# Performance work log

Measured on AMD Instinct MI355X. Metric: run time of the kernel, lower is better.

The kernel has to match this reference:

```python
import jax, jax.numpy as jnp
import numpy as np
import math

HIDDEN = 768
HEADS = 12
HEAD_DIM = HIDDEN // HEADS
B, S = 2, 4096


def setup_inputs() -> dict:
    key = jax.random.key(0)
    ks = jax.random.split(key, 12)
    scale = 1.0 / math.sqrt(HIDDEN)
    inp = {
        "key": jax.random.normal(ks[0], (B, S, HIDDEN), jnp.float32),
        "value": jax.random.normal(ks[1], (B, S, HIDDEN), jnp.float32),
        "query": jax.random.normal(ks[2], (B, S, HIDDEN), jnp.float32),
        "mask": jnp.zeros((B, 1, S, S), jnp.float32),
        # weights stored as [in, out] so projection is x @ W + b
        "Wq": jax.random.normal(ks[3], (HIDDEN, HIDDEN), jnp.float32) * scale,
        "bq": jnp.zeros((HIDDEN,), jnp.float32),
        "Wk": jax.random.normal(ks[4], (HIDDEN, HIDDEN), jnp.float32) * scale,
        "bk": jnp.zeros((HIDDEN,), jnp.float32),
        "Wv": jax.random.normal(ks[5], (HIDDEN, HIDDEN), jnp.float32) * scale,
        "bv": jnp.zeros((HIDDEN,), jnp.float32),
        "Wo": jax.random.normal(ks[6], (HIDDEN, HIDDEN), jnp.float32) * scale,
        "bo": jnp.zeros((HIDDEN,), jnp.float32),
    }
    return inp


def reference(key, value, query, mask, Wq, bq, Wk, bk, Wv, bv, Wo, bo):
    b, s, h = key.shape
    def proj(x, W, bias):
        # [b,s,h] -> [b, heads, s, head_dim]
        y = jnp.dot(x, W) + bias
        return y.reshape(b, s, HEADS, HEAD_DIM).transpose(0, 2, 1, 3)

    q = proj(query, Wq, bq)
    k = proj(key, Wk, bk)
    v = proj(value, Wv, bv)

    inv_sqrt_d = 1.0 / math.sqrt(float(HEAD_DIM))
    scores = jnp.einsum("bnqd,bnkd->bnqk", q, k) * inv_sqrt_d + mask
    probs = jax.nn.softmax(scores, axis=-1)  # dropout p=0.0 -> identity
    ctx = jnp.einsum("bnqk,bnkd->bnqd", probs, v)
    ctx = ctx.transpose(0, 2, 1, 3).reshape(b, s, h)
    return jnp.dot(ctx, Wo) + bo
```

## Files before the change

### kernel.cpp

```cpp
#include <hip/hip_runtime.h>
#include <hip/hip_bf16.h>

#define HID 768
#define NH 12
#define HD 64
#define BB 2
#define SS 4096
#define MM (BB*SS)

typedef unsigned short u16;
typedef __attribute__((ext_vector_type(8))) short short8;
typedef __attribute__((ext_vector_type(8))) unsigned short u16x8;
typedef __attribute__((ext_vector_type(4))) float f32x4;
typedef __attribute__((ext_vector_type(16))) float f32x16;

__device__ __forceinline__ u16 f2bf(float f) {
  union { float f; unsigned u; } v; v.f = f;
  return (u16)((v.u + 0x7fffu + ((v.u >> 16) & 1u)) >> 16);
}

__device__ __forceinline__ unsigned cvtpk(float lo, float hi) {
  unsigned r;
  asm("v_cvt_pk_bf16_f32 %0, %1, %2" : "=v"(r) : "v"(lo), "v"(hi));
  return r;
}

__device__ __forceinline__ short8 mk8(unsigned a, unsigned b, unsigned c, unsigned d) {
  union { unsigned u[4]; short8 s; } x;
  x.u[0] = a; x.u[1] = b; x.u[2] = c; x.u[3] = d;
  return x.s;
}

__global__ void mask_scan(const uint4* __restrict__ m, long long n4, int* __restrict__ flag) {
  long long i = (long long)blockIdx.x * blockDim.x + threadIdx.x;
  long long stride = (long long)gridDim.x * blockDim.x;
  unsigned acc = 0;
  for (; i < n4; i += stride) {
    uint4 v = m[i];
    acc |= v.x | v.y | v.z | v.w;
  }
  if (__any(acc != 0)) {
    if ((threadIdx.x & 63) == 0) atomicOr(flag, 1);
  }
}

__global__ void w_transpose(const float* __restrict__ w0, const float* __restrict__ w1,
                            const float* __restrict__ w2, const float* __restrict__ w3,
                            u16* __restrict__ wt) {
  const float* W = (blockIdx.z == 0) ? w0 : (blockIdx.z == 1) ? w1 : (blockIdx.z == 2) ? w2 : w3;
  u16* Wt = wt + (size_t)blockIdx.z * HID * HID;
  __shared__ float tile[64][65];
  int kb = blockIdx.x * 64, nb = blockIdx.y * 64;
  int t = threadIdx.x;
  int r = t >> 2, cg = (t & 3) << 4;
  const float* src = W + (size_t)(kb + r) * HID + nb + cg;
#pragma unroll
  for (int i = 0; i < 4; i++) {
    float4 v = *(const float4*)(src + 4 * i);
    tile[r][cg + 4*i + 0] = v.x;
    tile[r][cg + 4*i + 1] = v.y;
    tile[r][cg + 4*i + 2] = v.z;
    tile[r][cg + 4*i + 3] = v.w;
  }
  __syncthreads();
  u16x8 a, b;
#pragma unroll
  for (int i = 0; i < 8; i++) a[i] = f2bf(tile[cg + i][r]);
#pragma unroll
  for (int i = 0; i < 8; i++) b[i] = f2bf(tile[cg + 8 + i][r]);
  u16* dst = Wt + (size_t)(nb + r) * HID + kb + cg;
  *(u16x8*)dst = a;
  *(u16x8*)(dst + 8) = b;
}

__global__ void v_transpose(const u16* __restrict__ v_bf, u16* __restrict__ vt_bf) {
  int bh = blockIdx.y, sb = blockIdx.x * 64;
  __shared__ u16 tile[64][72];
  const u16* src = v_bf + (size_t)bh * SS * HD;
  u16* dst = vt_bf + (size_t)bh * HD * SS;
  int t = threadIdx.x;
  int r = t >> 2, cg = (t & 3) << 4;
  *(u16x8*)(&tile[r][cg])     = *(const u16x8*)(src + (size_t)(sb + r) * HD + cg);
  *(u16x8*)(&tile[r][cg + 8]) = *(const u16x8*)(src + (size_t)(sb + r) * HD + cg + 8);
  __syncthreads();
  u16x8 a, b;
#pragma unroll
  for (int i = 0; i < 8; i++) a[i] = tile[cg + i][r];
#pragma unroll
  for (int i = 0; i < 8; i++) b[i] = tile[cg + 8 + i][r];
  *(u16x8*)(dst + (size_t)r * SS + sb + cg) = a;
  *(u16x8*)(dst + (size_t)r * SS + sb + cg + 8) = b;
}

__launch_bounds__(256)
__global__ void proj_qkv(const float* __restrict__ Xq, const float* __restrict__ Xk,
                         const float* __restrict__ Xv, const u16* __restrict__ wt,
                         const float* __restrict__ bq, const float* __restrict__ bk,
                         const float* __restrict__ bv,
                         u16* __restrict__ qo, u16* __restrict__ ko, u16* __restrict__ vo) {
  int which = blockIdx.z;
  const float* X   = which == 0 ? Xq : which == 1 ? Xk : Xv;
  const u16* Wt    = wt + (size_t)which * HID * HID;
  const float* bias = which == 0 ? bq : which == 1 ? bk : bv;
  u16* out         = which == 0 ? qo : which == 1 ? ko : vo;

  __shared__ u16 Al[128 * 40];
  __shared__ u16 Bl[128 * 40];
  int t = threadIdx.x;
  int mbase = blockIdx.x * 128, nbase = blockIdx.y * 128;
  int wid = t >> 6, lane = t & 63, g = lane >> 4, c = lane & 15;
  int wm = wid >> 1, wn = wid & 1;

  f32x4 acc[4][4];
#pragma unroll
  for (int i = 0; i < 4; i++)
#pragma unroll
    for (int j = 0; j < 4; j++) acc[i][j] = 0.0f;

  int ar = t >> 1, ac = (t & 1) << 4;
  const float* xrow = X  + (size_t)(mbase + ar) * HID + ac;
  const u16*   wrow = Wt + (size_t)(nbase + ar) * HID + ac;
  u16* adst = &Al[ar * 40 + ac];
  u16* bdst = &Bl[ar * 40 + ac];

  for (int k0 = 0; k0 < HID; k0 += 32) {
    float4 x0 = *(const float4*)(xrow + k0);
    float4 x1 = *(const float4*)(xrow + k0 + 4);
    float4 x2 = *(const float4*)(xrow + k0 + 8);
    float4 x3 = *(const float4*)(xrow + k0 + 12);
    u16x8 pa_, pb_;
    pa_[0]=f2bf(x0.x); pa_[1]=f2bf(x0.y); pa_[2]=f2bf(x0.z); pa_[3]=f2bf(x0.w);
    pa_[4]=f2bf(x1.x); pa_[5]=f2bf(x1.y); pa_[6]=f2bf(x1.z); pa_[7]=f2bf(x1.w);
    pb_[0]=f2bf(x2.x); pb_[1]=f2bf(x2.y); pb_[2]=f2bf(x2.z); pb_[3]=f2bf(x2.w);
    pb_[4]=f2bf(x3.x); pb_[5]=f2bf(x3.y); pb_[6]=f2bf(x3.z); pb_[7]=f2bf(x3.w);
    u16x8 w0 = *(const u16x8*)(wrow + k0);
    u16x8 w1 = *(const u16x8*)(wrow + k0 + 8);
    *(u16x8*)adst       = pa_;
    *(u16x8*)(adst + 8) = pb_;
    *(u16x8*)bdst       = w0;
    *(u16x8*)(bdst + 8) = w1;
    __syncthreads();
    short8 af[4], bfr[4];
#pragma unroll
    for (int i = 0; i < 4; i++)
      af[i] = *(const short8*)(&Al[(wm*64 + i*16 + c) * 40 + 8*g]);
#pragma unroll
    for (int i = 0; i < 4; i++)
      bfr[i] = *(const short8*)(&Bl[(wn*64 + i*16 + c) * 40 + 8*g]);
#pragma unroll
    for (int mi = 0; mi < 4; mi++)
#pragma unroll
      for (int ni = 0; ni < 4; ni++)
        acc[mi][ni] = __builtin_amdgcn_mfma_f32_16x16x32_bf16(af[mi], bfr[ni], acc[mi][ni], 0, 0, 0);
    __syncthreads();
  }
#pragma unroll
  for (int ni = 0; ni < 4; ni++) {
    int n = nbase + wn*64 + ni*16 + c;
    float bv_ = bias[n];
    int hh = n >> 6, dd = n & 63;
#pragma unroll
    for (int mi = 0; mi < 4; mi++)
#pragma unroll
      for (int j = 0; j < 4; j++) {
        int m = mbase + wm*64 + mi*16 + 4*g + j;
        int bidx = m >> 12, s_ = m & (SS - 1);
        out[(((size_t)bidx * NH + hh) * SS + s_) * HD + dd] = f2bf(acc[mi][ni][j] + bv_);
      }
  }
}

__launch_bounds__(256)
__global__ void proj_out(const u16* __restrict__ X, const u16* __restrict__ Wt,
                         const float* __restrict__ bias, float* __restrict__ out) {
  __shared__ u16 Al[128 * 40];
  __shared__ u16 Bl[128 * 40];
  int t = threadIdx.x;
  int mbase = blockIdx.x * 128, nbase = blockIdx.y * 128;
  int wid = t >> 6, lane = t & 63, g = lane >> 4, c = lane & 15;
  int wm = wid >> 1, wn = wid & 1;

  f32x4 acc[4][4];
#pragma unroll
  for (int i = 0; i < 4; i++)
#pragma unroll
    for (int j = 0; j < 4; j++) acc[i][j] = 0.0f;

  int ar = t >> 1, ac = (t & 1) << 4;
  const u16* xrow = X  + (size_t)(mbase + ar) * HID + ac;
  const u16* wrow = Wt + (size_t)(nbase + ar) * HID + ac;
  u16* adst = &Al[ar * 40 + ac];
  u16* bdst = &Bl[ar * 40 + ac];

  for (int k0 = 0; k0 < HID; k0 += 32) {
    u16x8 a0 = *(const u16x8*)(xrow + k0);
    u16x8 a1 = *(const u16x8*)(xrow + k0 + 8);
    u16x8 w0 = *(const u16x8*)(wrow + k0);
    u16x8 w1 = *(const u16x8*)(wrow + k0 + 8);
    *(u16x8*)adst       = a0;
    *(u16x8*)(adst + 8) = a1;
    *(u16x8*)bdst       = w0;
    *(u16x8*)(bdst + 8) = w1;
    __syncthreads();
    short8 af[4], bfr[4];
#pragma unroll
    for (int i = 0; i < 4; i++)
      af[i] = *(const short8*)(&Al[(wm*64 + i*16 + c) * 40 + 8*g]);
#pragma unroll
    for (int i = 0; i < 4; i++)
      bfr[i] = *(const short8*)(&Bl[(wn*64 + i*16 + c) * 40 + 8*g]);
#pragma unroll
    for (int mi = 0; mi < 4; mi++)
#pragma unroll
      for (int ni = 0; ni < 4; ni++)
        acc[mi][ni] = __builtin_amdgcn_mfma_f32_16x16x32_bf16(af[mi], bfr[ni], acc[mi][ni], 0, 0, 0);
    __syncthreads();
  }
#pragma unroll
  for (int ni = 0; ni < 4; ni++) {
    int n = nbase + wn*64 + ni*16 + c;
    float bv_ = bias[n];
#pragma unroll
    for (int mi = 0; mi < 4; mi++)
#pragma unroll
      for (int j = 0; j < 4; j++) {
        int m = mbase + wm*64 + mi*16 + 4*g + j;
        out[(size_t)m * HID + n] = acc[mi][ni][j] + bv_;
      }
  }
}

__launch_bounds__(256)
__global__ void attn(const u16* __restrict__ q_bf, const u16* __restrict__ k_bf,
                     const u16* __restrict__ vt_bf, const float* __restrict__ mask,
                     const int* __restrict__ flag, u16* __restrict__ ctx) {
  const int qb = blockIdx.x, bh = blockIdx.y;
  const int b = bh / NH, hh = bh - b * NH;
  const u16* Q  = q_bf  + (size_t)bh * SS * HD;
  const u16* K  = k_bf  + (size_t)bh * SS * HD;
  const u16* VT = vt_bf + (size_t)bh * HD * SS;
  const int t = threadIdx.x, wid = t >> 6, lane = t & 63;
  const int c5 = lane & 31, h2 = lane >> 5;
  const int qbase = qb * 128 + wid * 32;
  const int use_mask = *flag;

  __shared__ u16 KV[2 * 8192];

  short8 qf0, qf1, qf2, qf3;
  {
    const u16* qrow = Q + (size_t)(qbase + c5) * HD + 8 * h2;
    qf0 = *(const short8*)(qrow);
    qf1 = *(const short8*)(qrow + 16);
    qf2 = *(const short8*)(qrow + 32);
    qf3 = *(const short8*)(qrow + 48);
  }

  f32x16 o0, o1; o0 = 0.0f; o1 = 0.0f;
  float m_run = -1e30f, l_run = 0.0f;

  const int sr = t >> 2, sq = t & 3;
  const int o_k0 = sr * 64 + (((2 * sq) ^ (sr & 7)) * 8);
  const u16* kp = K  + (size_t)sr * HD + sq * 16;
  const u16* vp = VT + (size_t)sr * SS + sq * 16;
  u16x8 rk0 = *(const u16x8*)kp, rk1 = *(const u16x8*)(kp + 8);
  u16x8 rv0 = *(const u16x8*)vp, rv1 = *(const u16x8*)(vp + 8);

  const int sw = c5 & 7;
  const int krow0 = c5 * 64, krow1 = (32 + c5) * 64;

  for (int tl = 0; tl < SS / 64; ++tl) {
    const int bufo = (tl & 1) * 8192;
    u16* kd = KV + bufo;
    *(u16x8*)(kd + o_k0)              = rk0;
    *(u16x8*)(kd + (o_k0 ^ 8))        = rk1;
    *(u16x8*)(kd + 4096 + o_k0)       = rv0;
    *(u16x8*)(kd + 4096 + (o_k0 ^ 8)) = rv1;
    if (tl < SS / 64 - 1) {
      kp += 64 * HD; vp += 64;
      rk0 = *(const u16x8*)kp; rk1 = *(const u16x8*)(kp + 8);
      rv0 = *(const u16x8*)vp; rv1 = *(const u16x8*)(vp + 8);
    }
    __syncthreads();
    const u16* Kb = KV + bufo;
    const u16* Vb = KV + bufo + 4096;

    f32x16 s0, s1; s0 = 0.0f; s1 = 0.0f;
#pragma unroll
    for (int dc = 0; dc < 4; ++dc) {
      short8 qv = dc == 0 ? qf0 : dc == 1 ? qf1 : dc == 2 ? qf2 : qf3;
      short8 ka = *(const short8*)(Kb + krow0 + (((2 * dc + h2) ^ sw) * 8));
      s0 = __builtin_amdgcn_mfma_f32_32x32x16_bf16(ka, qv, s0, 0, 0, 0);
    }
#pragma unroll
    for (int dc = 0; dc < 4; ++dc) {
      short8 qv = dc == 0 ? qf0 : dc == 1 ? qf1 : dc == 2 ? qf2 : qf3;
      short8 ka = *(const short8*)(Kb + krow1 + (((2 * dc + h2) ^ sw) * 8));
      s1 = __builtin_amdgcn_mfma_f32_32x32x16_bf16(ka, qv, s1, 0, 0, 0);
    }

    if (use_mask) {
      const float* mrow = mask + ((size_t)b * SS + (qbase + c5)) * SS + (size_t)tl * 64;
#pragma unroll
      for (int j = 0; j < 16; ++j) {
        const int row = (j & 3) + 8 * (j >> 2) + 4 * h2;
        s0[j] = fmaf(mrow[row],      8.0f, s0[j]);
        s1[j] = fmaf(mrow[32 + row], 8.0f, s1[j]);
      }
    }

    float rm = fmaxf(s0[0], s1[0]);
#pragma unroll
    for (int j = 1; j < 16; ++j) rm = fmaxf(rm, fmaxf(s0[j], s1[j]));
    rm = fmaxf(rm, __shfl_xor(rm, 32));
    const float pmax = rm * 0.125f;

    if (!__all(pmax <= m_run + 8.0f)) {
      const float mn = fmaxf(m_run, pmax);
      const float ef = __expf(m_run - mn);
      m_run = mn; l_run *= ef;
#pragma unroll
      for (int j = 0; j < 16; ++j) {
        const int row = (j & 3) + 8 * (j >> 2) + 4 * h2;
        const float eb = __shfl(ef, row);
        o0[j] *= eb; o1[j] *= eb;
      }
    }

    float ts = 0.0f;
#pragma unroll
    for (int j = 0; j < 16; ++j) { float p = __expf(fmaf(s0[j], 0.125f, -m_run)); s0[j] = p; ts += p; }
#pragma unroll
    for (int j = 0; j < 16; ++j) { float p = __expf(fmaf(s1[j], 0.125f, -m_run)); s1[j] = p; ts += p; }
    ts += __shfl_xor(ts, 32);
    l_run += ts;

    unsigned w00 = cvtpk(s0[0],  s0[1]),  w01 = cvtpk(s0[2],  s0[3]);
    unsigned w10 = cvtpk(s0[4],  s0[5]),  w11 = cvtpk(s0[6],  s0[7]);
    unsigned w20 = cvtpk(s0[8],  s0[9]),  w21 = cvtpk(s0[10], s0[11]);
    unsigned w30 = cvtpk(s0[12], s0[13]), w31 = cvtpk(s0[14], s0[15]);
    unsigned y00 = cvtpk(s1[0],  s1[1]),  y01 = cvtpk(s1[2],  s1[3]);
    unsigned y10 = cvtpk(s1[4],  s1[5]),  y11 = cvtpk(s1[6],  s1[7]);
    unsigned y20 = cvtpk(s1[8],  s1[9]),  y21 = cvtpk(s1[10], s1[11]);
    unsigned y30 = cvtpk(s1[12], s1[13]), y31 = cvtpk(s1[14], s1[15]);

    unsigned x1 = __shfl_xor(h2 ? w00 : w10, 32);
    unsigned x2 = __shfl_xor(h2 ? w01 : w11, 32);
    unsigned x3 = __shfl_xor(h2 ? w20 : w30, 32);
    unsigned x4 = __shfl_xor(h2 ? w21 : w31, 32);
    unsigned x5 = __shfl_xor(h2 ? y00 : y10, 32);
    unsigned x6 = __shfl_xor(h2 ? y01 : y11, 32);
    unsigned x7 = __shfl_xor(h2 ? y20 : y30, 32);
    unsigned x8 = __shfl_xor(h2 ? y21 : y31, 32);
    short8 p0 = mk8(h2 ? x1 : w00, h2 ? x2 : w01, h2 ? w10 : x1, h2 ? w11 : x2);
    short8 p1 = mk8(h2 ? x3 : w20, h2 ? x4 : w21, h2 ? w30 : x3, h2 ? w31 : x4);
    short8 p2 = mk8(h2 ? x5 : y00, h2 ? x6 : y01, h2 ? y10 : x5, h2 ? y11 : x6);
    short8 p3 = mk8(h2 ? x7 : y20, h2 ? x8 : y21, h2 ? y30 : x7, h2 ? y31 : x8);

#pragma unroll
    for (int kc = 0; kc < 4; ++kc) {
      short8 pa = kc == 0 ? p0 : kc == 1 ? p1 : kc == 2 ? p2 : p3;
      short8 v0 = *(const short8*)(Vb + krow0 + (((2 * kc + h2) ^ sw) * 8));
      o0 = __builtin_amdgcn_mfma_f32_32x32x16_bf16(pa, v0, o0, 0, 0, 0);
      short8 v1 = *(const short8*)(Vb + krow1 + (((2 * kc + h2) ^ sw) * 8));
      o1 = __builtin_amdgcn_mfma_f32_32x32x16_bf16(pa, v1, o1, 0, 0, 0);
    }
  }

  const float inv = 1.0f / l_run;
  u16* cbase = ctx + ((size_t)b * SS) * HID + hh * HD;
#pragma unroll
  for (int j = 0; j < 16; ++j) {
    const int row = (j & 3) + 8 * (j >> 2) + 4 * h2;
    const float ib = __shfl(inv, row);
    u16* crow = cbase + (size_t)(qbase + row) * HID;
    crow[c5]      = f2bf(o0[j] * ib);
    crow[32 + c5] = f2bf(o1[j] * ib);
  }
}

extern "C" void kernel_launch(void* const* d_in, const int* in_sizes, int n_in,
                              void* d_out, int out_size, void* d_ws, size_t ws_size,
                              hipStream_t stream) {
  (void)in_sizes; (void)n_in; (void)out_size; (void)ws_size;
  const float* key   = (const float*)d_in[0];
  const float* value = (const float*)d_in[1];
  const float* query = (const float*)d_in[2];
  const float* mask  = (const float*)d_in[3];
  const float* Wq = (const float*)d_in[4];
  const float* bq = (const float*)d_in[5];
  const float* Wk = (const float*)d_in[6];
  const float* bk = (const float*)d_in[7];
  const float* Wv = (const float*)d_in[8];
  const float* bv = (const float*)d_in[9];
  const float* Wo = (const float*)d_in[10];
  const float* bo = (const float*)d_in[11];

  char* ws = (char*)d_ws;
  const size_t WSZ = (size_t)HID * HID * 2;
  const size_t QSZ = (size_t)BB * NH * SS * HD * 2;
  u16* w_t   = (u16*)ws;
  u16* q_bf  = (u16*)(ws + 4*WSZ);
  u16* k_bf  = (u16*)(ws + 4*WSZ + QSZ);
  u16* v_bf  = (u16*)(ws + 4*WSZ + 2*QSZ);
  u16* vt_bf = (u16*)(ws + 4*WSZ + 3*QSZ);
  u16* ctx   = (u16*)(ws + 4*WSZ + 4*QSZ);
  int* flag  = (int*)(ws + 4*WSZ + 5*QSZ);

  hipMemsetAsync(flag, 0, 4, stream);
  mask_scan<<<2048, 256, 0, stream>>>((const uint4*)mask, (long long)BB*SS*SS/4, flag);
  w_transpose<<<dim3(12, 12, 4), 256, 0, stream>>>(Wq, Wk, Wv, Wo, w_t);
  proj_qkv<<<dim3(MM/128, HID/128, 3), 256, 0, stream>>>(query, key, value, w_t,
                                                         bq, bk, bv, q_bf, k_bf, v_bf);
  v_transpose<<<dim3(SS/64, BB*NH), 256, 0, stream>>>(v_bf, vt_bf);
  attn<<<dim3(SS/128, BB*NH), 256, 0, stream>>>(q_bf, k_bf, vt_bf, mask, flag, ctx);
  proj_out<<<dim3(MM/128, HID/128), 256, 0, stream>>>(ctx, w_t + 3*(size_t)HID*HID, bo,
                                                      (float*)d_out);
}
```

Baseline: 551.9 us.

## Use permlane32 swaps, exp2-domain softmax, and setprio around MFMA blocks

Replaces the ds_bpermute-based cross-half shuffles (max, sum, and the P fragment exchange) with v_permlane32_swap, which removes LDS traffic and selects. It also folds the 1/sqrt(d) scale and log2(e) into a single constant so the softmax uses exp2 directly, rescaling the lazy-rescale threshold to match. Finally it raises wave priority around the QK and PV MFMA blocks to encourage overlap between waves. The permlane intrinsic is specific to gfx950, and exp2f may compile to a slower path unless it lowers to the native instruction.

Measured after the change: 578.5 us. 1.05x slower.

```diff
diff --git a/kernel.cpp b/kernel.cpp
--- a/kernel.cpp
+++ b/kernel.cpp
@@ -1,5 +1,6 @@
 #include <hip/hip_runtime.h>
 #include <hip/hip_bf16.h>
+#include <math.h>
 
 #define HID 768
 #define NH 12
@@ -30,6 +31,26 @@
   x.u[0] = a; x.u[1] = b; x.u[2] = c; x.u[3] = d;
   return x.s;
 }
+
+__device__ __forceinline__ void pls(unsigned &a, unsigned &b) {
+  typedef __attribute__((ext_vector_type(2))) unsigned uv2;
+  uv2 r = __builtin_amdgcn_permlane32_swap(a, b, false, false);
+  a = r[0]; b = r[1];
+}
+
+__device__ __forceinline__ float swap_max(float x) {
+  union { float f; unsigned u; } a, b; a.f = x; b.f = x;
+  pls(a.u, b.u);
+  return fmaxf(a.f, b.f);
+}
+__device__ __forceinline__ float swap_add(float x) {
+  union { float f; unsigned u; } a, b; a.f = x; b.f = x;
+  pls(a.u, b.u);
+  return a.f + b.f;
+}
+
+#define C2F 0.18033688f
+#define THR2 11.5415603f
 
 __global__ void mask_scan(const uint4* __restrict__ m, long long n4, int* __restrict__ flag) {
   long long i = (long long)blockIdx.x * blockDim.x + threadIdx.x;
@@ -256,7 +277,7 @@
   }
 
   f32x16 o0, o1; o0 = 0.0f; o1 = 0.0f;
-  float m_run = -1e30f, l_run = 0.0f;
+  float m2_run = -1e30f, l_run = 0.0f;
 
   const int sr = t >> 2, sq = t & 3;
   const int o_k0 = sr * 64 + (((2 * sq) ^ (sr & 7)) * 8);
@@ -285,6 +306,7 @@
     const u16* Vb = KV + bufo + 4096;
 
     f32x16 s0, s1; s0 = 0.0f; s1 = 0.0f;
+    __builtin_amdgcn_s_setprio(1);
 #pragma unroll
     for (int dc = 0; dc < 4; ++dc) {
       short8 qv = dc == 0 ? qf0 : dc == 1 ? qf1 : dc == 2 ? qf2 : qf3;
@@ -297,6 +319,7 @@
       short8 ka = *(const short8*)(Kb + krow1 + (((2 * dc + h2) ^ sw) * 8));
       s1 = __builtin_amdgcn_mfma_f32_32x32x16_bf16(ka, qv, s1, 0, 0, 0);
     }
+    __builtin_amdgcn_s_setprio(0);
 
     if (use_mask) {
       const float* mrow = mask + ((size_t)b * SS + (qbase + c5)) * SS + (size_t)tl * 64;
@@ -311,13 +334,12 @@
     float rm = fmaxf(s0[0], s1[0]);
 #pragma unroll
     for (int j = 1; j < 16; ++j) rm = fmaxf(rm, fmaxf(s0[j], s1[j]));
-    rm = fmaxf(rm, __shfl_xor(rm, 32));
-    const float pmax = rm * 0.125f;
-
-    if (!__all(pmax <= m_run + 8.0f)) {
-      const float mn = fmaxf(m_run, pmax);
-      const float ef = __expf(m_run - mn);
-      m_run = mn; l_run *= ef;
+    const float pmax2 = swap_max(rm) * C2F;
+
+    if (!__all(pmax2 <= m2_run + THR2)) {
+      const float mn = fmaxf(m2_run, pmax2);
+      const float ef = exp2f(m2_run - mn);
+      m2_run = mn; l_run *= ef;
 #pragma unroll
       for (int j = 0; j < 16; ++j) {
         const int row = (j & 3) + 8 * (j >> 2) + 4 * h2;
@@ -328,11 +350,10 @@
 
     float ts = 0.0f;
 #pragma unroll
-    for (int j = 0; j < 16; ++j) { float p = __expf(fmaf(s0[j], 0.125f, -m_run)); s0[j] = p; ts += p; }
-#pragma unroll
-    for (int j = 0; j < 16; ++j) { float p = __expf(fmaf(s1[j], 0.125f, -m_run)); s1[j] = p; ts += p; }
-    ts += __shfl_xor(ts, 32);
-    l_run += ts;
+    for (int j = 0; j < 16; ++j) { float p = exp2f(fmaf(s0[j], C2F, -m2_run)); s0[j] = p; ts += p; }
+#pragma unroll
+    for (int j = 0; j < 16; ++j) { float p = exp2f(fmaf(s1[j], C2F, -m2_run)); s1[j] = p; ts += p; }
+    l_run += swap_add(ts);
 
     unsigned w00 = cvtpk(s0[0],  s0[1]),  w01 = cvtpk(s0[2],  s0[3]);
     unsigned w10 = cvtpk(s0[4],  s0[5]),  w11 = cvtpk(s0[6],  s0[7]);
@@ -343,19 +364,16 @@
     unsigned y20 = cvtpk(s1[8],  s1[9]),  y21 = cvtpk(s1[10], s1[11]);
     unsigned y30 = cvtpk(s1[12], s1[13]), y31 = cvtpk(s1[14], s1[15]);
 
-    unsigned x1 = __shfl_xor(h2 ? w00 : w10, 32);
-    unsigned x2 = __shfl_xor(h2 ? w01 : w11, 32);
-    unsigned x3 = __shfl_xor(h2 ? w20 : w30, 32);
-    unsigned x4 = __shfl_xor(h2 ? w21 : w31, 32);
-    unsigned x5 = __shfl_xor(h2 ? y00 : y10, 32);
-    unsigned x6 = __shfl_xor(h2 ? y01 : y11, 32);
-    unsigned x7 = __shfl_xor(h2 ? y20 : y30, 32);
-    unsigned x8 = __shfl_xor(h2 ? y21 : y31, 32);
-    short8 p0 = mk8(h2 ? x1 : w00, h2 ? x2 : w01, h2 ? w10 : x1, h2 ? w11 : x2);
-    short8 p1 = mk8(h2 ? x3 : w20, h2 ? x4 : w21, h2 ? w30 : x3, h2 ? w31 : x4);
-    short8 p2 = mk8(h2 ? x5 : y00, h2 ? x6 : y01, h2 ? y10 : x5, h2 ? y11 : x6);
-    short8 p3 = mk8(h2 ? x7 : y20, h2 ? x8 : y21, h2 ? y30 : x7, h2 ? y31 : x8);
-
+    pls(w00, w10); pls(w01, w11);
+    pls(w20, w30); pls(w21, w31);
+    pls(y00, y10); pls(y01, y11);
+    pls(y20, y30); pls(y21, y31);
+    short8 p0 = mk8(w00, w01, w10, w11);
+    short8 p1 = mk8(w20, w21, w30, w31);
+    short8 p2 = mk8(y00, y01, y10, y11);
+    short8 p3 = mk8(y20, y21, y30, y31);
+
+    __builtin_amdgcn_s_setprio(1);
 #pragma unroll
     for (int kc = 0; kc < 4; ++kc) {
       short8 pa = kc == 0 ? p0 : kc == 1 ? p1 : kc == 2 ? p2 : p3;
@@ -364,6 +382,7 @@
       short8 v1 = *(const short8*)(Vb + krow1 + (((2 * kc + h2) ^ sw) * 8));
       o1 = __builtin_amdgcn_mfma_f32_32x32x16_bf16(pa, v1, o1, 0, 0, 0);
     }
+    __builtin_amdgcn_s_setprio(0);
   }
 
   const float inv = 1.0f / l_run;
```
